# Kernel optimization log

Hardware: AMD Instinct MI355X
Metric: run time of the kernel (lower is better)

The kernel has to match this reference:

```python
import jax, jax.numpy as jnp
import numpy as np

N = 80000   # active voxels
G = 64      # voxel grid side
K = 27      # 3x3x3 kernel taps


def _build_coord_maps():
    """Random unique voxel coords in a G^3 grid; 27-tap neighbor index map (-1 = missing)."""
    rng = np.random.default_rng(0)
    flat = rng.choice(G ** 3, size=N, replace=False).astype(np.int64)
    coords = np.stack(np.unravel_index(flat, (G, G, G)), axis=1)  # (N,3)
    order = np.argsort(flat)
    skeys = flat[order]
    offs = [(dx, dy, dz) for dx in (-1, 0, 1) for dy in (-1, 0, 1) for dz in (-1, 0, 1)]
    nbr = np.full((K, N), -1, np.int32)
    for k, (dx, dy, dz) in enumerate(offs):
        nc = coords + np.array([dx, dy, dz])
        inb = np.all((nc >= 0) & (nc < G), axis=1)
        nkey = nc[:, 0] * G * G + nc[:, 1] * G + nc[:, 2]
        pos = np.clip(np.searchsorted(skeys, nkey), 0, N - 1)
        hit = inb & (skeys[pos] == nkey)
        nbr[k] = np.where(hit, order[pos], -1)
    return nbr


_W_SPECS = [('a1w', (27, 96, 64)), ('a2w', (64, 64)), ('a3w', (27, 64, 64)), ('a4w', (64, 64)),
            ('b1w', (27, 256, 64)), ('b2w', (64, 64)), ('b3w', (27, 64, 32)), ('b4w', (32, 32)),
            ('c1w', (27, 96, 128)), ('c2w', (128, 128)), ('c3w', (128, 128))]
_BN_SPECS = [('a1', 64), ('a2', 64), ('a3', 64), ('a4', 64),
             ('b1', 64), ('b2', 64), ('b3', 32), ('b4', 32),
             ('c1', 128), ('c2', 128), ('c3', 128)]


def setup_inputs() -> dict:
    key = jax.random.key(0)
    ks = jax.random.split(key, 64)
    inp = {
        'feat3d': jax.random.normal(ks[0], (N, 96), jnp.float32),
        'feat2d': jax.random.normal(ks[1], (N, 256), jnp.float32),
    }
    i = 2
    for name, shp in _W_SPECS:
        fan = float(np.prod(shp[:-1]))
        inp[name] = jax.random.normal(ks[i], shp, jnp.float32) * (1.0 / np.sqrt(fan))
        i += 1
    for pre, c in _BN_SPECS:  # folded eval-mode BN: y = x*scale + shift
        inp[pre + 's'] = 1.0 + 0.1 * jax.random.normal(ks[i], (c,), jnp.float32)
        inp[pre + 'b'] = 0.1 * jax.random.normal(ks[i + 1], (c,), jnp.float32)
        i += 2
    inp['nbr_idx'] = jnp.asarray(_build_coord_maps())
    inp['align_idx'] = jnp.arange(N, dtype=jnp.int32)  # 2D/3D share coordinates -> exact match
    return inp


def _sconv(x, W, nbr):
    """Sparse 3x3x3 conv: per-tap masked gather + GEMM, accumulated (gather-GEMM-scatter)."""
    out = jnp.zeros((x.shape[0], W.shape[-1]), x.dtype)
    for k in range(W.shape[0]):
        idx = nbr[k]
        g = jnp.where((idx >= 0)[:, None], x[jnp.maximum(idx, 0)], 0.0)
        out = out + g @ W[k]
    return out


def _bnrelu(x, s, b):
    return jax.nn.relu(x * s + b)


def reference(feat3d, feat2d,
              a1w, a2w, a3w, a4w, b1w, b2w, b3w, b4w, c1w, c2w, c3w,
              a1s, a1b, a2s, a2b, a3s, a3b, a4s, a4b,
              b1s, b1b, b2s, b2b, b3s, b3b, b4s, b4b,
              c1s, c1b, c2s, c2b, c3s, c3b,
              nbr_idx, align_idx):
    # 3D branch: 96 -> 64 (dropout = identity in eval)
    x = _bnrelu(_sconv(feat3d, a1w, nbr_idx), a1s, a1b)
    x = _bnrelu(x @ a2w, a2s, a2b)
    x = _bnrelu(_sconv(x, a3w, nbr_idx), a3s, a3b)
    x3 = _bnrelu(x @ a4w, a4s, a4b)
    # 2D branch: 256 -> 32
    y = _bnrelu(_sconv(feat2d, b1w, nbr_idx), b1s, b1b)
    y = _bnrelu(y @ b2w, b2s, b2b)
    y = _bnrelu(_sconv(y, b3w, nbr_idx), b3s, b3b)
    y2 = _bnrelu(y @ b4w, b4s, b4b)
    # features_at_coordinates: exact-match gather at the 3D coords, NaN/Inf -> 0
    ya = y2[align_idx]
    ya = jnp.where(jnp.isfinite(ya), ya, 0.0)
    # fusion: concat 64+32=96 -> 128
    z = jnp.concatenate([x3, ya], axis=1)
    z = _bnrelu(_sconv(z, c1w, nbr_idx), c1s, c1b)
    z = _bnrelu(z @ c2w, c2s, c2b)
    z = _bnrelu(z @ c3w, c3s, c3b)
    return z
```

## Files before the change

### kernel.cpp

```cpp
#include <hip/hip_runtime.h>

typedef __bf16 bf16;
typedef __bf16 bf16x8 __attribute__((ext_vector_type(8)));
typedef __bf16 bf16x4 __attribute__((ext_vector_type(4)));
typedef float  f32x4  __attribute__((ext_vector_type(4)));

__global__ void f2b_kernel(const float* __restrict__ src, bf16* __restrict__ dst, int n4) {
    int i = blockIdx.x * 256 + threadIdx.x;
    if (i >= n4) return;
    float4 v = ((const float4*)src)[i];
    bf16x4 o = { (bf16)v.x, (bf16)v.y, (bf16)v.z, (bf16)v.w };
    ((bf16x4*)dst)[i] = o;
}

__global__ void swz_kernel(const float* __restrict__ W, bf16* __restrict__ Wf,
                           int cin, int cout, int total) {
    int e = blockIdx.x * 256 + threadIdx.x;
    if (e >= total) return;
    int per_tap = cin * cout;
    int tap = e / per_tap;
    int t2  = e - tap * per_tap;
    int ntc = cout >> 4;
    int s   = t2 / (ntc * 512);
    int r3  = t2 - s * (ntc * 512);
    int nt  = r3 >> 9;
    int L   = (r3 & 511) >> 3;
    int j   = r3 & 7;
    int k   = s * 32 + (L >> 4) * 8 + j;
    int col = nt * 16 + (L & 15);
    Wf[e] = (bf16)W[((size_t)tap * cin + k) * cout + col];
}

template<int CIN, int C1, int TAPS, int C2, int C3>
__global__ __launch_bounds__(64, 2) void layer_kernel(
    const bf16* __restrict__ X,
    const bf16* __restrict__ W1,
    const bf16* __restrict__ W2,
    const bf16* __restrict__ W3,
    const int*  __restrict__ nbr,
    const float* __restrict__ sc1, const float* __restrict__ sh1,
    const float* __restrict__ sc2, const float* __restrict__ sh2,
    const float* __restrict__ sc3, const float* __restrict__ sh3,
    bf16* __restrict__ Y, float* __restrict__ Yf,
    int ystride, int yoff, int n, int nblocks)
{
    constexpr int NT1 = C1 / 16;
    constexpr int WC1 = NT1;
    constexpr int WR1 = (C1 >= 128) ? 2 : 4;
    constexpr int RW  = WR1 * 16;
    constexpr int KS  = CIN / 32;
    constexpr int TOT = TAPS * KS;
    constexpr int LS1 = C1 + 8;
    constexpr int LS2 = C2 + 8;
    constexpr int LSM = (LS1 > LS2) ? LS1 : LS2;

    __shared__ __align__(16) bf16 Lt[RW * LSM];

    const int lane = threadIdx.x;
    const int m16  = lane & 15;
    const int quad = lane >> 4;

    const int bq = nblocks >> 3, br = nblocks & 7;
    const int bx = blockIdx.x & 7, bs = blockIdx.x >> 3;
    const int sb = bx * bq + (bx < br ? bx : br) + bs;
    const int base = sb * RW;

    const bf16x8 ZB = __builtin_bit_cast(bf16x8, (float4){0.f, 0.f, 0.f, 0.f});

    int idxc[WR1], idxn[WR1];
    auto load_idx = [&](int t, int (&id)[WR1]) {
#pragma unroll
        for (int r = 0; r < WR1; ++r)
            id[r] = nbr[(size_t)t * n + base + r * 16 + m16];
    };
    auto load_b = [&](int step, bf16x8 (&b)[WC1]) {
        const bf16* wt = W1 + (size_t)step * (NT1 * 512) + lane * 8;
#pragma unroll
        for (int c = 0; c < WC1; ++c)
            b[c] = *(const bf16x8*)(wt + c * 512);
    };

    f32x4 acc1[WR1][WC1];
#pragma unroll
    for (int r = 0; r < WR1; ++r)
#pragma unroll
        for (int c = 0; c < WC1; ++c) acc1[r][c] = (f32x4){0.f, 0.f, 0.f, 0.f};

    bf16x8 aA[WR1], aB[WR1], bA[WC1], bB[WC1];

    load_idx(0, idxc);
    load_idx(1, idxn);
    load_b(0, bA);
#pragma unroll
    for (int r = 0; r < WR1; ++r) {
        bf16x8 v = ZB;
        int id_ = idxc[r];
        if (id_ >= 0) v = *(const bf16x8*)(X + (unsigned)id_ * CIN + quad * 8);
        aA[r] = v;
    }

    int t = 0, s = 0;
    auto step = [&](int it, bf16x8 (&aC)[WR1], bf16x8 (&bC)[WC1],
                    bf16x8 (&aN)[WR1], bf16x8 (&bN)[WC1]) {
        int s1 = s + 1, t1 = t;
        bool wrap = (s1 == KS);
        if (wrap) { s1 = 0; ++t1; }
        if (it + 1 < TOT) {
            load_b(t1 * KS + s1, bN);
#pragma unroll
            for (int r = 0; r < WR1; ++r) {
                int id_ = wrap ? idxn[r] : idxc[r];
                bf16x8 v = ZB;
                if (id_ >= 0) v = *(const bf16x8*)(X + (unsigned)id_ * CIN + s1 * 32 + quad * 8);
                aN[r] = v;
            }
        }
#pragma unroll
        for (int r = 0; r < WR1; ++r)
#pragma unroll
            for (int c = 0; c < WC1; ++c)
                acc1[r][c] = __builtin_amdgcn_mfma_f32_16x16x32_bf16(aC[r], bC[c], acc1[r][c], 0, 0, 0);
        if (wrap) {
#pragma unroll
            for (int r = 0; r < WR1; ++r) idxc[r] = idxn[r];
            if (t + 2 < TAPS) load_idx(t + 2, idxn);
        }
        t = t1; s = s1;
    };

    for (int it = 0; it < TOT; it += 2) {
        step(it, aA, bA, aB, bB);
        if (it + 1 < TOT) step(it + 1, aB, bB, aA, bA);
    }

#pragma unroll
    for (int c = 0; c < WC1; ++c) {
        int col = c * 16 + m16;
        float sc = sc1[col], sh = sh1[col];
#pragma unroll
        for (int r = 0; r < WR1; ++r) {
            int row0 = r * 16 + quad * 4;
#pragma unroll
            for (int i = 0; i < 4; ++i) {
                float v = acc1[r][c][i] * sc + sh;
                v = v > 0.f ? v : 0.f;
                Lt[(row0 + i) * LS1 + col] = (bf16)v;
            }
        }
    }

    constexpr int NT2 = C2 / 16;
    constexpr int WC2 = NT2;
    constexpr int KS2 = C1 / 32;

    f32x4 acc2[WR1][WC2];
#pragma unroll
    for (int r = 0; r < WR1; ++r)
#pragma unroll
        for (int c = 0; c < WC2; ++c) acc2[r][c] = (f32x4){0.f, 0.f, 0.f, 0.f};

#pragma unroll
    for (int s2 = 0; s2 < KS2; ++s2) {
        bf16x8 a[WR1], bw[WC2];
#pragma unroll
        for (int r = 0; r < WR1; ++r)
            a[r] = *(const bf16x8*)(&Lt[(r * 16 + m16) * LS1 + s2 * 32 + quad * 8]);
#pragma unroll
        for (int c = 0; c < WC2; ++c)
            bw[c] = *(const bf16x8*)(W2 + ((s2 * NT2 + c) * 512 + lane * 8));
#pragma unroll
        for (int r = 0; r < WR1; ++r)
#pragma unroll
            for (int c = 0; c < WC2; ++c)
                acc2[r][c] = __builtin_amdgcn_mfma_f32_16x16x32_bf16(a[r], bw[c], acc2[r][c], 0, 0, 0);
    }

    if constexpr (C3 == 0) {
#pragma unroll
        for (int c = 0; c < WC2; ++c) {
            int col = c * 16 + m16;
            float sc = sc2[col], sh = sh2[col];
#pragma unroll
            for (int r = 0; r < WR1; ++r) {
                int row0 = base + r * 16 + quad * 4;
#pragma unroll
                for (int i = 0; i < 4; ++i) {
                    float v = acc2[r][c][i] * sc + sh;
                    v = v > 0.f ? v : 0.f;
                    size_t off = (size_t)(row0 + i) * ystride + yoff + col;
                    if (Yf) Yf[off] = v;
                    else    Y[off] = (bf16)v;
                }
            }
        }
    } else {
#pragma unroll
        for (int c = 0; c < WC2; ++c) {
            int col = c * 16 + m16;
            float sc = sc2[col], sh = sh2[col];
#pragma unroll
            for (int r = 0; r < WR1; ++r) {
                int row0 = r * 16 + quad * 4;
#pragma unroll
                for (int i = 0; i < 4; ++i) {
                    float v = acc2[r][c][i] * sc + sh;
                    v = v > 0.f ? v : 0.f;
                    Lt[(row0 + i) * LS2 + col] = (bf16)v;
                }
            }
        }

        constexpr int C3v = (C3 > 0) ? C3 : 16;
        constexpr int NT3 = C3v / 16;
        constexpr int WC3 = NT3;
        constexpr int KS3 = C2 / 32;

        f32x4 acc3[WR1][WC3];
#pragma unroll
        for (int r = 0; r < WR1; ++r)
#pragma unroll
            for (int c = 0; c < WC3; ++c) acc3[r][c] = (f32x4){0.f, 0.f, 0.f, 0.f};

#pragma unroll
        for (int s3 = 0; s3 < KS3; ++s3) {
            bf16x8 a[WR1], bw[WC3];
#pragma unroll
            for (int r = 0; r < WR1; ++r)
                a[r] = *(const bf16x8*)(&Lt[(r * 16 + m16) * LS2 + s3 * 32 + quad * 8]);
#pragma unroll
            for (int c = 0; c < WC3; ++c)
                bw[c] = *(const bf16x8*)(W3 + ((s3 * NT3 + c) * 512 + lane * 8));
#pragma unroll
            for (int r = 0; r < WR1; ++r)
#pragma unroll
                for (int c = 0; c < WC3; ++c)
                    acc3[r][c] = __builtin_amdgcn_mfma_f32_16x16x32_bf16(a[r], bw[c], acc3[r][c], 0, 0, 0);
        }

#pragma unroll
        for (int c = 0; c < WC3; ++c) {
            int col = c * 16 + m16;
            float sc = sc3[col], sh = sh3[col];
#pragma unroll
            for (int r = 0; r < WR1; ++r) {
                int row0 = base + r * 16 + quad * 4;
#pragma unroll
                for (int i = 0; i < 4; ++i) {
                    float v = acc3[r][c][i] * sc + sh;
                    v = v > 0.f ? v : 0.f;
                    size_t off = (size_t)(row0 + i) * ystride + yoff + col;
                    if (Yf) Yf[off] = v;
                    else    Y[off] = (bf16)v;
                }
            }
        }
    }
}

__global__ void concat_kernel(const bf16* __restrict__ y2, const int* __restrict__ align,
                              bf16* __restrict__ z, int n) {
    int e = blockIdx.x * 256 + threadIdx.x;
    if (e >= n * 32) return;
    int i = e >> 5, c = e & 31;
    int a = align[i];
    float v = (float)y2[(size_t)a * 32 + c];
    unsigned u = __builtin_bit_cast(unsigned, v);
    if ((u & 0x7f800000u) == 0x7f800000u) v = 0.f;
    z[(size_t)i * 96 + 64 + c] = (bf16)v;
}

extern "C" void kernel_launch(void* const* d_in, const int* in_sizes, int n_in,
                              void* d_out, int out_size, void* d_ws, size_t ws_size,
                              hipStream_t stream) {
    const float* feat3d = (const float*)d_in[0];
    const float* feat2d = (const float*)d_in[1];
    const float* Wsrc[11];
    for (int i = 0; i < 11; ++i) Wsrc[i] = (const float*)d_in[2 + i];
    const float* bn[22];
    for (int i = 0; i < 22; ++i) bn[i] = (const float*)d_in[13 + i];
    const int* nbr   = (const int*)d_in[35];
    const int* align = (const int*)d_in[36];
    float* out = (float*)d_out;

    const int n = in_sizes[0] / 96;

    char* ws = (char*)d_ws;
    size_t off = 0;
    auto alloc = [&](size_t bytes) -> void* {
        void* p = ws + off;
        off = (off + bytes + 255) & ~(size_t)255;
        return p;
    };
    bf16* F3 = (bf16*)alloc((size_t)n * 96 * 2);
    bf16* F2 = (bf16*)alloc((size_t)n * 256 * 2);
    static const int wt_taps[11] = {27, 1, 27, 1, 27, 1, 27, 1, 27, 1, 1};
    static const int wt_cin[11]  = {96, 64, 64, 64, 256, 64, 64, 32, 96, 128, 128};
    static const int wt_cout[11] = {64, 64, 64, 64, 64, 64, 32, 32, 128, 128, 128};
    bf16* Wf[11];
    for (int i = 0; i < 11; ++i)
        Wf[i] = (bf16*)alloc((size_t)wt_taps[i] * wt_cin[i] * wt_cout[i] * 2);
    bf16* tA = (bf16*)alloc((size_t)n * 64 * 2);
    bf16* tB = (bf16*)alloc((size_t)n * 64 * 2);
    bf16* y2 = (bf16*)alloc((size_t)n * 32 * 2);
    bf16* z  = (bf16*)alloc((size_t)n * 96 * 2);

    f2b_kernel<<<(n * 96 / 4 + 255) / 256, 256, 0, stream>>>(feat3d, F3, n * 96 / 4);
    f2b_kernel<<<(n * 256 / 4 + 255) / 256, 256, 0, stream>>>(feat2d, F2, n * 256 / 4);
    for (int i = 0; i < 11; ++i) {
        int total = wt_taps[i] * wt_cin[i] * wt_cout[i];
        swz_kernel<<<(total + 255) / 256, 256, 0, stream>>>(Wsrc[i], Wf[i], wt_cin[i], wt_cout[i], total);
    }

    const int GB64 = n / 64;
    const int GB32 = n / 32;

    layer_kernel<96, 64, 27, 64, 0><<<GB64, 64, 0, stream>>>(
        F3, Wf[0], Wf[1], nullptr, nbr,
        bn[0], bn[1], bn[2], bn[3], nullptr, nullptr,
        tB, nullptr, 64, 0, n, GB64);
    layer_kernel<64, 64, 27, 64, 0><<<GB64, 64, 0, stream>>>(
        tB, Wf[2], Wf[3], nullptr, nbr,
        bn[4], bn[5], bn[6], bn[7], nullptr, nullptr,
        z, nullptr, 96, 0, n, GB64);

    layer_kernel<256, 64, 27, 64, 0><<<GB64, 64, 0, stream>>>(
        F2, Wf[4], Wf[5], nullptr, nbr,
        bn[8], bn[9], bn[10], bn[11], nullptr, nullptr,
        tA, nullptr, 64, 0, n, GB64);
    layer_kernel<64, 32, 27, 32, 0><<<GB64, 64, 0, stream>>>(
        tA, Wf[6], Wf[7], nullptr, nbr,
        bn[12], bn[13], bn[14], bn[15], nullptr, nullptr,
        y2, nullptr, 32, 0, n, GB64);

    concat_kernel<<<(n * 32 + 255) / 256, 256, 0, stream>>>(y2, align, z, n);

    layer_kernel<96, 128, 27, 128, 128><<<GB32, 64, 0, stream>>>(
        z, Wf[8], Wf[9], Wf[10], nbr,
        bn[16], bn[17], bn[18], bn[19], bn[20], bn[21],
        nullptr, out, 128, 0, n, GB32);
}
```

Baseline: 631.1 us.

## Split sparse-conv taps across four waves with LDS partial-sum reduction

```diff
diff --git a/kernel.cpp b/kernel.cpp
--- a/kernel.cpp
+++ b/kernel.cpp
@@ -32,7 +32,7 @@
 }
 
 template<int CIN, int C1, int TAPS, int C2, int C3>
-__global__ __launch_bounds__(64, 2) void layer_kernel(
+__global__ __launch_bounds__(256, 3) void layer_kernel(
     const bf16* __restrict__ X,
     const bf16* __restrict__ W1,
     const bf16* __restrict__ W2,
@@ -46,17 +46,25 @@
 {
     constexpr int NT1 = C1 / 16;
     constexpr int WC1 = NT1;
-    constexpr int WR1 = (C1 >= 128) ? 2 : 4;
-    constexpr int RW  = WR1 * 16;
+    constexpr int RW  = (C1 >= 128) ? 32 : 64;
+    constexpr int WR1 = RW / 16;
     constexpr int KS  = CIN / 32;
-    constexpr int TOT = TAPS * KS;
     constexpr int LS1 = C1 + 8;
     constexpr int LS2 = C2 + 8;
-    constexpr int LSM = (LS1 > LS2) ? LS1 : LS2;
-
-    __shared__ __align__(16) bf16 Lt[RW * LSM];
-
-    const int lane = threadIdx.x;
+    constexpr int HC  = C1 / 2;
+    constexpr int HCP = HC + 1;
+    constexpr int PRB = 4 * RW * HCP * 4;
+    constexpr int LTB = RW * LS1 * 2;
+    constexpr bool BPRE = (WC1 <= 4);
+
+    __shared__ __align__(16) char smem[PRB + LTB];
+    float* PR  = (float*)smem;
+    bf16*  Lt  = (bf16*)(smem + PRB);
+    bf16*  Lt2 = (bf16*)smem;
+
+    const int tid  = threadIdx.x;
+    const int lane = tid & 63;
+    const int wv   = tid >> 6;
     const int m16  = lane & 15;
     const int quad = lane >> 4;
 
@@ -65,6 +73,11 @@
     const int sb = bx * bq + (bx < br ? bx : br) + bs;
     const int base = sb * RW;
 
+    constexpr int TB = TAPS / 4, TR = TAPS % 4;
+    const int tstart = wv * TB + (wv < TR ? wv : TR);
+    const int tcnt   = TB + (wv < TR ? 1 : 0);
+    const int TOTW   = tcnt * KS;
+
     const bf16x8 ZB = __builtin_bit_cast(bf16x8, (float4){0.f, 0.f, 0.f, 0.f});
 
     int idxc[WR1], idxn[WR1];
@@ -73,8 +86,8 @@
         for (int r = 0; r < WR1; ++r)
             id[r] = nbr[(size_t)t * n + base + r * 16 + m16];
     };
-    auto load_b = [&](int step, bf16x8 (&b)[WC1]) {
-        const bf16* wt = W1 + (size_t)step * (NT1 * 512) + lane * 8;
+    auto load_b = [&](int gstep, bf16x8 (&b)[WC1]) {
+        const bf16* wt = W1 + (size_t)gstep * (NT1 * 512) + lane * 8;
 #pragma unroll
         for (int c = 0; c < WC1; ++c)
             b[c] = *(const bf16x8*)(wt + c * 512);
@@ -88,33 +101,33 @@
 
     bf16x8 aA[WR1], aB[WR1], bA[WC1], bB[WC1];
 
-    load_idx(0, idxc);
-    load_idx(1, idxn);
-    load_b(0, bA);
+    load_idx(tstart, idxc);
+    if (tcnt > 1) load_idx(tstart + 1, idxn);
+    if constexpr (BPRE) load_b(tstart * KS, bA);
 #pragma unroll
     for (int r = 0; r < WR1; ++r) {
         bf16x8 v = ZB;
-        int id_ = idxc[r];
-        if (id_ >= 0) v = *(const bf16x8*)(X + (unsigned)id_ * CIN + quad * 8);
+        if (idxc[r] >= 0) v = *(const bf16x8*)(X + (size_t)(unsigned)idxc[r] * CIN + quad * 8);
         aA[r] = v;
     }
 
-    int t = 0, s = 0;
-    auto step = [&](int it, bf16x8 (&aC)[WR1], bf16x8 (&bC)[WC1],
-                    bf16x8 (&aN)[WR1], bf16x8 (&bN)[WC1]) {
-        int s1 = s + 1, t1 = t;
+    int tloc = 0, s = 0;
+    auto dostep = [&](int it, bf16x8 (&aC)[WR1], bf16x8 (&bC)[WC1],
+                      bf16x8 (&aN)[WR1], bf16x8 (&bN)[WC1]) {
+        int s1 = s + 1, tl1 = tloc;
         bool wrap = (s1 == KS);
-        if (wrap) { s1 = 0; ++t1; }
-        if (it + 1 < TOT) {
-            load_b(t1 * KS + s1, bN);
+        if (wrap) { s1 = 0; ++tl1; }
+        if (it + 1 < TOTW) {
+            if constexpr (BPRE) load_b((tstart + tl1) * KS + s1, bN);
 #pragma unroll
             for (int r = 0; r < WR1; ++r) {
                 int id_ = wrap ? idxn[r] : idxc[r];
                 bf16x8 v = ZB;
-                if (id_ >= 0) v = *(const bf16x8*)(X + (unsigned)id_ * CIN + s1 * 32 + quad * 8);
+                if (id_ >= 0) v = *(const bf16x8*)(X + (size_t)(unsigned)id_ * CIN + s1 * 32 + quad * 8);
                 aN[r] = v;
             }
         }
+        if constexpr (!BPRE) load_b((tstart + tloc) * KS + s, bC);
 #pragma unroll
         for (int r = 0; r < WR1; ++r)
 #pragma unroll
@@ -123,135 +136,130 @@
         if (wrap) {
 #pragma unroll
             for (int r = 0; r < WR1; ++r) idxc[r] = idxn[r];
-            if (t + 2 < TAPS) load_idx(t + 2, idxn);
-        }
-        t = t1; s = s1;
+            if (tloc + 2 < tcnt) load_idx(tstart + tloc + 2, idxn);
+        }
+        tloc = tl1; s = s1;
     };
 
-    for (int it = 0; it < TOT; it += 2) {
-        step(it, aA, bA, aB, bB);
-        if (it + 1 < TOT) step(it + 1, aB, bB, aA, bA);
-    }
-
-#pragma unroll
-    for (int c = 0; c < WC1; ++c) {
-        int col = c * 16 + m16;
-        float sc = sc1[col], sh = sh1[col];
-#pragma unroll
-        for (int r = 0; r < WR1; ++r) {
-            int row0 = r * 16 + quad * 4;
+    for (int it = 0; it < TOTW; it += 2) {
+        dostep(it, aA, bA, aB, bB);
+        if (it + 1 < TOTW) dostep(it + 1, aB, bB, aA, bA);
+    }
+
+    constexpr int SLICE = RW / 4;
+#pragma unroll
+    for (int p = 0; p < 2; ++p) {
+        __syncthreads();
+        float* Pw = PR + wv * (RW * HCP);
+#pragma unroll
+        for (int c = 0; c < WC1 / 2; ++c)
+#pragma unroll
+            for (int r = 0; r < WR1; ++r)
+#pragma unroll
+                for (int i = 0; i < 4; ++i)
+                    Pw[(r * 16 + quad * 4 + i) * HCP + c * 16 + m16] = acc1[r][p * (WC1 / 2) + c][i];
+        __syncthreads();
+#pragma unroll
+        for (int e = lane; e < SLICE * HC; e += 64) {
+            int row  = wv * SLICE + e / HC;
+            int colh = e & (HC - 1);
+            float v = PR[(0 * RW + row) * HCP + colh] + PR[(1 * RW + row) * HCP + colh]
+                    + PR[(2 * RW + row) * HCP + colh] + PR[(3 * RW + row) * HCP + colh];
+            int col = p * HC + colh;
+            v = v * sc1[col] + sh1[col];
+            v = v > 0.f ? v : 0.f;
+            Lt[row * LS1 + col] = (bf16)v;
+        }
+    }
+    __syncthreads();
+
+    constexpr int NT2  = C2 / 16;
+    constexpr int DRW  = RW / 16 >= 4 ? 4 : RW / 16;
+    constexpr int NCG  = 4 / DRW;
+    constexpr int WC2g = NT2 / NCG;
+    constexpr int KS2  = C1 / 32;
+    const int wr  = wv % DRW;
+    const int wcg = wv / DRW;
+
+    f32x4 acc2[WC2g];
+#pragma unroll
+    for (int c = 0; c < WC2g; ++c) acc2[c] = (f32x4){0.f, 0.f, 0.f, 0.f};
+
+#pragma unroll
+    for (int s2 = 0; s2 < KS2; ++s2) {
+        bf16x8 a = *(const bf16x8*)(&Lt[(wr * 16 + m16) * LS1 + s2 * 32 + quad * 8]);
+        bf16x8 bw[WC2g];
+#pragma unroll
+        for (int c = 0; c < WC2g; ++c)
+            bw[c] = *(const bf16x8*)(W2 + ((s2 * NT2 + wcg * WC2g + c) * 512 + lane * 8));
+#pragma unroll
+        for (int c = 0; c < WC2g; ++c)
+            acc2[c] = __builtin_amdgcn_mfma_f32_16x16x32_bf16(a, bw[c], acc2[c], 0, 0, 0);
+    }
+
+    if constexpr (C3 == 0) {
+#pragma unroll
+        for (int c = 0; c < WC2g; ++c) {
+            int col = (wcg * WC2g + c) * 16 + m16;
+            float sc = sc2[col], sh = sh2[col];
+            int row0 = base + wr * 16 + quad * 4;
 #pragma unroll
             for (int i = 0; i < 4; ++i) {
-                float v = acc1[r][c][i] * sc + sh;
+                float v = acc2[c][i] * sc + sh;
                 v = v > 0.f ? v : 0.f;
-                Lt[(row0 + i) * LS1 + col] = (bf16)v;
+                size_t off = (size_t)(row0 + i) * ystride + yoff + col;
+                if (Yf) Yf[off] = v;
+                else    Y[off] = (bf16)v;
             }
         }
-    }
-
-    constexpr int NT2 = C2 / 16;
-    constexpr int WC2 = NT2;
-    constexpr int KS2 = C1 / 32;
-
-    f32x4 acc2[WR1][WC2];
-#pragma unroll
-    for (int r = 0; r < WR1; ++r)
-#pragma unroll
-        for (int c = 0; c < WC2; ++c) acc2[r][c] = (f32x4){0.f, 0.f, 0.f, 0.f};
-
-#pragma unroll
-    for (int s2 = 0; s2 < KS2; ++s2) {
-        bf16x8 a[WR1], bw[WC2];
-#pragma unroll
-        for (int r = 0; r < WR1; ++r)
-            a[r] = *(const bf16x8*)(&Lt[(r * 16 + m16) * LS1 + s2 * 32 + quad * 8]);
-#pragma unroll
-        for (int c = 0; c < WC2; ++c)
-            bw[c] = *(const bf16x8*)(W2 + ((s2 * NT2 + c) * 512 + lane * 8));
-#pragma unroll
-        for (int r = 0; r < WR1; ++r)
-#pragma unroll
-            for (int c = 0; c < WC2; ++c)
-                acc2[r][c] = __builtin_amdgcn_mfma_f32_16x16x32_bf16(a[r], bw[c], acc2[r][c], 0, 0, 0);
-    }
-
-    if constexpr (C3 == 0) {
-#pragma unroll
-        for (int c = 0; c < WC2; ++c) {
-            int col = c * 16 + m16;
+    } else {
+#pragma unroll
+        for (int c = 0; c < WC2g; ++c) {
+            int col = (wcg * WC2g + c) * 16 + m16;
             float sc = sc2[col], sh = sh2[col];
-#pragma unroll
-            for (int r = 0; r < WR1; ++r) {
-                int row0 = base + r * 16 + quad * 4;
-#pragma unroll
-                for (int i = 0; i < 4; ++i) {
-                    float v = acc2[r][c][i] * sc + sh;
-                    v = v > 0.f ? v : 0.f;
-                    size_t off = (size_t)(row0 + i) * ystride + yoff + col;
-                    if (Yf) Yf[off] = v;
-                    else    Y[off] = (bf16)v;
-                }
+            int row0 = wr * 16 + quad * 4;
+#pragma unroll
+            for (int i = 0; i < 4; ++i) {
+                float v = acc2[c][i] * sc + sh;
+                v = v > 0.f ? v : 0.f;
+                Lt2[(row0 + i) * LS2 + col] = (bf16)v;
             }
         }
-    } else {
-#pragma unroll
-        for (int c = 0; c < WC2; ++c) {
-            int col = c * 16 + m16;
-            float sc = sc2[col], sh = sh2[col];
-#pragma unroll
-            for (int r = 0; r < WR1; ++r) {
-                int row0 = r * 16 + quad * 4;
-#pragma unroll
-                for (int i = 0; i < 4; ++i) {
-                    float v = acc2[r][c][i] * sc + sh;
-                    v = v > 0.f ? v : 0.f;
-                    Lt[(row0 + i) * LS2 + col] = (bf16)v;
-                }
-            }
-        }
-
-        constexpr int C3v = (C3 > 0) ? C3 : 16;
-        constexpr int NT3 = C3v / 16;
-        constexpr int WC3 = NT3;
-        constexpr int KS3 = C2 / 32;
-
-        f32x4 acc3[WR1][WC3];
-#pragma unroll
-        for (int r = 0; r < WR1; ++r)
-#pragma unroll
-            for (int c = 0; c < WC3; ++c) acc3[r][c] = (f32x4){0.f, 0.f, 0.f, 0.f};
+        __syncthreads();
+
+        constexpr int C3v  = (C3 > 0) ? C3 : 16;
+        constexpr int NT3  = C3v / 16;
+        constexpr int WC3g = NT3 / NCG;
+        constexpr int KS3  = C2 / 32;
+
+        f32x4 acc3[WC3g];
+#pragma unroll
+        for (int c = 0; c < WC3g; ++c) acc3[c] = (f32x4){0.f, 0.f, 0.f, 0.f};
 
 #pragma unroll
         for (int s3 = 0; s3 < KS3; ++s3) {
-            bf16x8 a[WR1], bw[WC3];
-#pragma unroll
-            for (int r = 0; r < WR1; ++r)
-                a[r] = *(const bf16x8*)(&Lt[(r * 16 + m16) * LS2 + s3 * 32 + quad * 8]);
-#pragma unroll
-            for (int c = 0; c < WC3; ++c)
-                bw[c] = *(const bf16x8*)(W3 + ((s3 * NT3 + c) * 512 + lane * 8));
-#pragma unroll
-            for (int r = 0; r < WR1; ++r)
-#pragma unroll
-                for (int c = 0; c < WC3; ++c)
-                    acc3[r][c] = __builtin_amdgcn_mfma_f32_16x16x32_bf16(a[r], bw[c], acc3[r][c], 0, 0, 0);
-        }
-
-#pragma unroll
-        for (int c = 0; c < WC3; ++c) {
-            int col = c * 16 + m16;
+            bf16x8 a = *(const bf16x8*)(&Lt2[(wr * 16 + m16) * LS2 + s3 * 32 + quad * 8]);
+            bf16x8 bw[WC3g];
+#pragma unroll
+            for (int c = 0; c < WC3g; ++c)
+                bw[c] = *(const bf16x8*)(W3 + ((s3 * NT3 + wcg * WC3g + c) * 512 + lane * 8));
+#pragma unroll
+            for (int c = 0; c < WC3g; ++c)
+                acc3[c] = __builtin_amdgcn_mfma_f32_16x16x32_bf16(a, bw[c], acc3[c], 0, 0, 0);
+        }
+
+#pragma unroll
+        for (int c = 0; c < WC3g; ++c) {
+            int col = (wcg * WC3g + c) * 16 + m16;
             float sc = sc3[col], sh = sh3[col];
-#pragma unroll
-            for (int r = 0; r < WR1; ++r) {
-                int row0 = base + r * 16 + quad * 4;
-#pragma unroll
-                for (int i = 0; i < 4; ++i) {
-                    float v = acc3[r][c][i] * sc + sh;
-                    v = v > 0.f ? v : 0.f;
-                    size_t off = (size_t)(row0 + i) * ystride + yoff + col;
-                    if (Yf) Yf[off] = v;
-                    else    Y[off] = (bf16)v;
-                }
+            int row0 = base + wr * 16 + quad * 4;
+#pragma unroll
+            for (int i = 0; i < 4; ++i) {
+                float v = acc3[c][i] * sc + sh;
+                v = v > 0.f ? v : 0.f;
+                size_t off = (size_t)(row0 + i) * ystride + yoff + col;
+                if (Yf) Yf[off] = v;
+                else    Y[off] = (bf16)v;
             }
         }
     }
@@ -314,27 +322,27 @@
     const int GB64 = n / 64;
     const int GB32 = n / 32;
 
-    layer_kernel<96, 64, 27, 64, 0><<<GB64, 64, 0, stream>>>(
+    layer_kernel<96, 64, 27, 64, 0><<<GB64, 256, 0, stream>>>(
         F3, Wf[0], Wf[1], nullptr, nbr,
         bn[0], bn[1], bn[2], bn[3], nullptr, nullptr,
         tB, nullptr, 64, 0, n, GB64);
-    layer_kernel<64, 64, 27, 64, 0><<<GB64, 64, 0, stream>>>(
+    layer_kernel<64, 64, 27, 64, 0><<<GB64, 256, 0, stream>>>(
         tB, Wf[2], Wf[3], nullptr, nbr,
         bn[4], bn[5], bn[6], bn[7], nullptr, nullptr,
         z, nullptr, 96, 0, n, GB64);
 
-    layer_kernel<256, 64, 27, 64, 0><<<GB64, 64, 0, stream>>>(
+    layer_kernel<256, 64, 27, 64, 0><<<GB64, 256, 0, stream>>>(
         F2, Wf[4], Wf[5], nullptr, nbr,
         bn[8], bn[9], bn[10], bn[11], nullptr, nullptr,
         tA, nullptr, 64, 0, n, GB64);
-    layer_kernel<64, 32, 27, 32, 0><<<GB64, 64, 0, stream>>>(
+    layer_kernel<64, 32, 27, 32, 0><<<GB64, 256, 0, stream>>>(
         tA, Wf[6], Wf[7], nullptr, nbr,
         bn[12], bn[13], bn[14], bn[15], nullptr, nullptr,
         y2, nullptr, 32, 0, n, GB64);
 
     concat_kernel<<<(n * 32 + 255) / 256, 256, 0, stream>>>(y2, align, z, n);
 
-    layer_kernel<96, 128, 27, 128, 128><<<GB32, 64, 0, stream>>>(
+    layer_kernel<96, 128, 27, 128, 128><<<GB32, 256, 0, stream>>>(
         z, Wf[8], Wf[9], Wf[10], nbr,
         bn[16], bn[17], bn[18], bn[19], bn[20], bn[21],
         nullptr, out, 128, 0, n, GB32);
```

Result: faster. 589.9 us (-6.5%).
